# Kernel optimization log

Hardware: AMD Instinct MI355X
Metric: run time of the kernel (lower is better)

Reference implementation:

```python
import jax, jax.numpy as jnp
import numpy as np

B, S, D = 2, 2048, 1024
H, DK, DV = 16, 64, 64
DF = 4096
EPS = 1e-5


def _layer_norm(x, g, b):
    mu = jnp.mean(x, axis=-1, keepdims=True)
    var = jnp.mean((x - mu) ** 2, axis=-1, keepdims=True)
    return (x - mu) * jax.lax.rsqrt(var + EPS) * g + b


def setup_inputs() -> dict:
    key = jax.random.key(0)
    ks = jax.random.split(key, 12)
    s = lambda fan_in: 1.0 / np.sqrt(fan_in)
    return {
        "enc_input": jax.random.normal(ks[0], (B, S, D), dtype=jnp.float32),
        "wq": jax.random.uniform(ks[1], (D, H * DK), jnp.float32, -s(D), s(D)),
        "wk": jax.random.uniform(ks[2], (D, H * DK), jnp.float32, -s(D), s(D)),
        "wv": jax.random.uniform(ks[3], (D, H * DV), jnp.float32, -s(D), s(D)),
        "wo": jax.random.uniform(ks[4], (H * DV, D), jnp.float32, -s(H * DV), s(H * DV)),
        "w1": jax.random.uniform(ks[5], (D, DF), jnp.float32, -s(D), s(D)),
        "b1": jax.random.uniform(ks[6], (DF,), jnp.float32, -s(D), s(D)),
        "w2": jax.random.uniform(ks[7], (DF, D), jnp.float32, -s(DF), s(DF)),
        "b2": jax.random.uniform(ks[8], (D,), jnp.float32, -s(DF), s(DF)),
        "ln1_g": jnp.ones((D,), jnp.float32),
        "ln1_b": jnp.zeros((D,), jnp.float32),
        "ln2_g": jnp.ones((D,), jnp.float32),
        "ln2_b": jnp.zeros((D,), jnp.float32),
    }


def reference(enc_input, wq, wk, wv, wo, w1, b1, w2, b2, ln1_g, ln1_b, ln2_g, ln2_b):
    x = enc_input
    # QKV projections -> [B, H, S, d]
    q = (x @ wq).reshape(B, S, H, DK).transpose(0, 2, 1, 3)
    k = (x @ wk).reshape(B, S, H, DK).transpose(0, 2, 1, 3)
    v = (x @ wv).reshape(B, S, H, DV).transpose(0, 2, 1, 3)
    # scaled dot-product attention (scale = 1/sqrt(d_k), dropout is identity at eval)
    score = jnp.einsum("bhqd,bhkd->bhqk", q, k) / jnp.sqrt(jnp.float32(DK))
    attn = jax.nn.softmax(score, axis=-1)
    ctx = jnp.einsum("bhqk,bhkd->bhqd", attn, v)
    ctx = ctx.transpose(0, 2, 1, 3).reshape(B, S, H * DV)
    atn_out = ctx @ wo
    # Add & Norm 1
    h = _layer_norm(x + atn_out, ln1_g, ln1_b)
    # FFN
    ffn = jax.nn.relu(h @ w1 + b1) @ w2 + b2
    # Add & Norm 2
    return _layer_norm(h + ffn, ln2_g, ln2_b)
```

## Files before the change

### kernel.cpp

```cpp
#include <hip/hip_runtime.h>
#include <hip/hip_bf16.h>

typedef __bf16 bf16;
typedef __bf16 bf16x4 __attribute__((ext_vector_type(4)));
typedef __bf16 bf16x8 __attribute__((ext_vector_type(8)));
typedef float  f32x4  __attribute__((ext_vector_type(4)));

#define KB 2
#define KS 2048
#define KD 1024
#define KH 16
#define KM (KB*KS)
#define KQKVN 3072
#define KDF 4096

__device__ __forceinline__ f32x4 mfma16(bf16x8 a, bf16x8 b, f32x4 c) {
  return __builtin_amdgcn_mfma_f32_16x16x32_bf16(a, b, c, 0, 0, 0);
}

__device__ __forceinline__ void g2l16(const bf16* g, bf16* l) {
  __builtin_amdgcn_global_load_lds(
      (const __attribute__((address_space(1))) unsigned int*)g,
      (__attribute__((address_space(3))) unsigned int*)l, 16, 0, 0);
}

__global__ __launch_bounds__(256) void cvt_bf16_kernel(const float* __restrict__ in,
                                                       bf16* __restrict__ out, int n) {
  int i = (blockIdx.x * 256 + threadIdx.x) * 4;
  if (i >= n) return;
  f32x4 v = *reinterpret_cast<const f32x4*>(in + i);
  bf16x4 o;
  o[0] = (bf16)v[0]; o[1] = (bf16)v[1]; o[2] = (bf16)v[2]; o[3] = (bf16)v[3];
  *reinterpret_cast<bf16x4*>(out + i) = o;
}

__global__ __launch_bounds__(256) void wtrans_kernel(const float* __restrict__ W,
                                                     bf16* __restrict__ WT,
                                                     int K, int N) {
  __shared__ float tile[32][33];
  const int n0 = blockIdx.x * 32, k0 = blockIdx.y * 32;
  const int tx = threadIdx.x & 31, ty = threadIdx.x >> 5;
#pragma unroll
  for (int j = ty; j < 32; j += 8) tile[j][tx] = W[(size_t)(k0 + j) * N + n0 + tx];
  __syncthreads();
#pragma unroll
  for (int j = ty; j < 32; j += 8) WT[(size_t)(n0 + j) * K + k0 + tx] = (bf16)tile[tx][j];
}

__global__ __launch_bounds__(256) void kvpack_kernel(const bf16* __restrict__ qkv,
                                                     bf16* __restrict__ kp,
                                                     bf16* __restrict__ vt) {
  __shared__ bf16 tile[64][72];
  const int s0 = blockIdx.x * 64;
  const int bh = blockIdx.y;
  const int b = bh >> 4, h = bh & 15;
  const int t = threadIdx.x;
  const int r = t >> 3, c8 = (t & 7) * 8;
#pragma unroll
  for (int rr = r; rr < 64; rr += 32) {
    const size_t grow = (size_t)(b * KS + s0 + rr) * KQKVN + h * 64 + c8;
    bf16x8 kv = *reinterpret_cast<const bf16x8*>(&qkv[grow + 1024]);
    *reinterpret_cast<bf16x8*>(&kp[((size_t)bh * KS + s0 + rr) * 64 + c8]) = kv;
    bf16x8 vv = *reinterpret_cast<const bf16x8*>(&qkv[grow + 2048]);
#pragma unroll
    for (int j = 0; j < 8; j++) tile[rr][c8 + j] = vv[j];
  }
  __syncthreads();
#pragma unroll
  for (int dd = r; dd < 64; dd += 32) {
    bf16x8 v;
#pragma unroll
    for (int j = 0; j < 8; j++) {
      const int pi = c8 + j;
      v[j] = tile[((pi & 3) << 4) + (pi >> 2)][dd];
    }
    *reinterpret_cast<bf16x8*>(&vt[(size_t)bh * 64 * KS + (size_t)dd * KS + s0 + c8]) = v;
  }
}

struct P4 { bf16* p[4]; };

template <typename OUT_T, bool RELU, bool HAS_BIAS, bool SPLITK>
__global__ __launch_bounds__(512, 2) void gemm256(const bf16* __restrict__ A,
                                                  const bf16* __restrict__ BT,
                                                  OUT_T* __restrict__ C, P4 pr,
                                                  const float* __restrict__ bias,
                                                  int M, int N, int K, int Kslice) {
  extern __shared__ __align__(16) bf16 sm[];
  const int tid = threadIdx.x, lane = tid & 63, w = tid >> 6;
  const int wr = w >> 2, wc = w & 3;
  const int gx = gridDim.x;
  const int nwg = gx * gridDim.y;
  int flat = blockIdx.y * gx + blockIdx.x;
  flat = (flat & 7) * (nwg >> 3) + (flat >> 3);
  const int bn = (flat % gx) * 256;
  const int bm = (flat / gx) * 256;
  const int z = blockIdx.z;
  const int NT = (SPLITK ? Kslice : K) >> 5;
  const int lr = lane & 15, hi = lane >> 4;
  int srow[2], scol[2];
#pragma unroll
  for (int j = 0; j < 2; j++) {
    const int u = j * 512 + tid;
    srow[j] = u >> 2;
    scol[j] = (((u & 3) ^ ((u >> 2) & 3))) * 8;
  }
  const bf16* Abase = A + (size_t)bm * K + (SPLITK ? z * Kslice : 0);
  const bf16* Bbase = BT + (size_t)bn * K + (SPLITK ? z * Kslice : 0);
  auto stage = [&](int t) {
    bf16* dst = sm + (size_t)(t & 3) * 16384;
    const int k0 = t * 32;
#pragma unroll
    for (int j = 0; j < 2; j++) {
      g2l16(Abase + (size_t)srow[j] * K + k0 + scol[j], dst + (j * 512 + w * 64) * 8);
      g2l16(Bbase + (size_t)srow[j] * K + k0 + scol[j],
            dst + 8192 + (j * 512 + w * 64) * 8);
    }
  };
  f32x4 acc[8][4] = {};
  stage(0); stage(1); stage(2);
  for (int t = 0; t < NT; t++) {
    const int rem = NT - 1 - t;
    if (rem >= 2)      asm volatile("s_waitcnt vmcnt(8)" ::: "memory");
    else if (rem == 1) asm volatile("s_waitcnt vmcnt(4)" ::: "memory");
    else               asm volatile("s_waitcnt vmcnt(0)" ::: "memory");
    __builtin_amdgcn_sched_barrier(0);
    __builtin_amdgcn_s_barrier();
    __builtin_amdgcn_sched_barrier(0);
    if (t + 3 < NT) stage(t + 3);
    const bf16* sa = sm + (size_t)(t & 3) * 16384;
    const bf16* sb = sa + 8192;
    bf16x8 af[8], bfr[4];
#pragma unroll
    for (int mf = 0; mf < 8; mf++) {
      const int row = wr * 128 + mf * 16 + lr;
      af[mf] = *(const bf16x8*)&sa[row * 32 + ((hi ^ (row & 3)) * 8)];
    }
#pragma unroll
    for (int nf = 0; nf < 4; nf++) {
      const int row = wc * 64 + nf * 16 + lr;
      bfr[nf] = *(const bf16x8*)&sb[row * 32 + ((hi ^ (row & 3)) * 8)];
    }
    __builtin_amdgcn_s_setprio(1);
#pragma unroll
    for (int mf = 0; mf < 8; mf++)
#pragma unroll
      for (int nf = 0; nf < 4; nf++)
        acc[mf][nf] = mfma16(af[mf], bfr[nf], acc[mf][nf]);
    __builtin_amdgcn_s_setprio(0);
  }
  const int rg = hi * 4, cl = lr;
  if (SPLITK) {
    bf16* P = pr.p[z];
#pragma unroll
    for (int mf = 0; mf < 8; mf++)
#pragma unroll
      for (int nf = 0; nf < 4; nf++) {
        const int col = bn + wc * 64 + nf * 16 + cl;
#pragma unroll
        for (int i = 0; i < 4; i++) {
          const int row = bm + wr * 128 + mf * 16 + rg + i;
          P[(size_t)row * N + col] = (bf16)acc[mf][nf][i];
        }
      }
  } else {
#pragma unroll
    for (int mf = 0; mf < 8; mf++)
#pragma unroll
      for (int nf = 0; nf < 4; nf++) {
        const int col = bn + wc * 64 + nf * 16 + cl;
        float bv = 0.f;
        if (HAS_BIAS) bv = bias[col];
#pragma unroll
        for (int i = 0; i < 4; i++) {
          const int row = bm + wr * 128 + mf * 16 + rg + i;
          float v = acc[mf][nf][i] + bv;
          if (RELU) v = fmaxf(v, 0.f);
          C[(size_t)row * N + col] = (OUT_T)v;
        }
      }
  }
}

__global__ __launch_bounds__(256) void ffn2_reduce_kernel(const bf16* __restrict__ p0,
                                                          const bf16* __restrict__ p1,
                                                          const bf16* __restrict__ p2,
                                                          const bf16* __restrict__ p3,
                                                          const float* __restrict__ b2,
                                                          float* __restrict__ out) {
  const size_t i = ((size_t)blockIdx.x * 256 + threadIdx.x) * 8;
  bf16x8 a0 = *(const bf16x8*)(p0 + i);
  bf16x8 a1 = *(const bf16x8*)(p1 + i);
  bf16x8 a2 = *(const bf16x8*)(p2 + i);
  bf16x8 a3 = *(const bf16x8*)(p3 + i);
  const int col = (int)(i & (KD - 1));
  f32x4 b0 = *(const f32x4*)(b2 + col);
  f32x4 b1 = *(const f32x4*)(b2 + col + 4);
  f32x4 o0, o1;
#pragma unroll
  for (int j = 0; j < 4; j++)
    o0[j] = (float)a0[j] + (float)a1[j] + (float)a2[j] + (float)a3[j] + b0[j];
#pragma unroll
  for (int j = 0; j < 4; j++)
    o1[j] = (float)a0[j + 4] + (float)a1[j + 4] + (float)a2[j + 4] + (float)a3[j + 4] + b1[j];
  *(f32x4*)(out + i) = o0;
  *(f32x4*)(out + i + 4) = o1;
}

template <typename OUT_T, bool RELU, bool HAS_BIAS, int BN>
__global__ __launch_bounds__(256) void gemm_bt(const bf16* __restrict__ A,
                                               const bf16* __restrict__ BT,
                                               OUT_T* __restrict__ C,
                                               const float* __restrict__ bias,
                                               int M, int N, int K) {
  constexpr int NF = BN / 32;
  __shared__ __align__(16) bf16 sa[2][128 * 32];
  __shared__ __align__(16) bf16 sb[2][BN * 32];
  const int t = threadIdx.x, lane = t & 63, w = t >> 6;
  const int gx = gridDim.x;
  const int nwg = gx * gridDim.y;
  int flat = blockIdx.y * gx + blockIdx.x;
  if ((nwg & 7) == 0) flat = (flat & 7) * (nwg >> 3) + (flat >> 3);
  const int bn = (flat % gx) * BN;
  const int bm = (flat / gx) * 128;
  const int wr = w >> 1, wc = w & 1;
  const int wcol = wc * (BN / 2);
  const int lr = lane & 15, lk = (lane >> 4) * 8;
  const int srow = w * 16 + (lane >> 2);
  const int scol = (lane & 3) * 8;
  f32x4 acc[4][NF] = {};
  const int NT = K >> 5;
  auto stage = [&](int kt, int buf) {
#pragma unroll
    for (int i = 0; i < 2; i++)
      g2l16(A + (size_t)(bm + i * 64 + srow) * K + kt * 32 + scol,
            &sa[buf][(i * 64 + w * 16) * 32]);
#pragma unroll
    for (int i = 0; i < BN / 64; i++)
      g2l16(BT + (size_t)(bn + i * 64 + srow) * K + kt * 32 + scol,
            &sb[buf][(i * 64 + w * 16) * 32]);
  };
  stage(0, 0);
  int cur = 0;
  for (int kt = 0; kt < NT; kt++) {
    __syncthreads();
    if (kt + 1 < NT) stage(kt + 1, cur ^ 1);
    bf16x8 af[4], bfr[NF];
#pragma unroll
    for (int m = 0; m < 4; m++)
      af[m] = *(const bf16x8*)&sa[cur][(wr * 64 + m * 16 + lr) * 32 + lk];
#pragma unroll
    for (int n = 0; n < NF; n++)
      bfr[n] = *(const bf16x8*)&sb[cur][(wcol + n * 16 + lr) * 32 + lk];
#pragma unroll
    for (int m = 0; m < 4; m++)
#pragma unroll
      for (int n = 0; n < NF; n++)
        acc[m][n] = mfma16(af[m], bfr[n], acc[m][n]);
    cur ^= 1;
  }
  const int rg = (lane >> 4) * 4, cl = lane & 15;
#pragma unroll
  for (int m = 0; m < 4; m++)
#pragma unroll
    for (int n = 0; n < NF; n++) {
      const int col = bn + wcol + n * 16 + cl;
      float bv = 0.f;
      if (HAS_BIAS) bv = bias[col];
#pragma unroll
      for (int i = 0; i < 4; i++) {
        const int row = bm + wr * 64 + m * 16 + rg + i;
        float v = acc[m][n][i] + bv;
        if (RELU) v = fmaxf(v, 0.f);
        C[(size_t)row * N + col] = (OUT_T)v;
      }
    }
}

__global__ __launch_bounds__(256) void attn_kernel(const bf16* __restrict__ qkv,
                                                   const bf16* __restrict__ kp,
                                                   const bf16* __restrict__ vt,
                                                   bf16* __restrict__ ctx) {
  __shared__ __align__(16) bf16 ksm[4][64 * 64];
  __shared__ __align__(16) bf16 vsm[4][64 * 64];
  __shared__ __align__(16) bf16 psm[4][32 * 64];
  const int t = threadIdx.x, lane = t & 63, w = t >> 6;
  const int flat = blockIdx.y * 16 + blockIdx.x;
  const int xcd = flat & 7, jj = flat >> 3;
  const int bh = xcd + 8 * (jj >> 4);
  const int qb = jj & 15;
  const int b = bh >> 4, h = bh & 15;
  const int qbase = qb * 128 + w * 32;
  const int lr = lane & 15, hi = lane >> 4;
  const int lk = hi * 8, rg = hi * 4, cl = lr;

  bf16x8 aq[2][2];
#pragma unroll
  for (int m = 0; m < 2; m++)
#pragma unroll
    for (int kk = 0; kk < 2; kk++) {
      bf16x8 v = *reinterpret_cast<const bf16x8*>(
          &qkv[(size_t)(b * KS + qbase + m * 16 + lr) * KQKVN + h * 64 + kk * 32 + lk]);
#pragma unroll
      for (int e = 0; e < 8; e++) v[e] = (bf16)((float)v[e] * 0.125f);
      aq[m][kk] = v;
    }

  const bf16* kpb = kp + (size_t)bh * KS * 64;
  const bf16* vtb = vt + (size_t)bh * 64 * KS;

  auto stageKV = [&](int tt) {
    const int kt0 = tt * 64;
    bf16* kd = &ksm[tt & 3][0];
    bf16* vd = &vsm[tt & 3][0];
#pragma unroll
    for (int i = 0; i < 2; i++) {
      const int q = i * 4096 + w * 1024 + (lane << 4);
      const int row = q >> 7;
      const int slot = ((q >> 4) & 7) ^ (row & 7);
      g2l16(kpb + (size_t)(kt0 + row) * 64 + slot * 8, kd + ((i * 4096 + w * 1024) >> 1));
      g2l16(vtb + (size_t)row * KS + kt0 + slot * 8,   vd + ((i * 4096 + w * 1024) >> 1));
    }
  };

  f32x4 accd[2][4] = {};
  float lsum[2][4] = {};

  stageKV(0); stageKV(1); stageKV(2);
  char* pb = (char*)&psm[w][0];
  const int NT = KS / 64;
  for (int tt = 0; tt < NT; tt++) {
    const int rem = NT - 1 - tt;
    if (rem >= 2)      asm volatile("s_waitcnt vmcnt(8)" ::: "memory");
    else if (rem == 1) asm volatile("s_waitcnt vmcnt(4)" ::: "memory");
    else               asm volatile("s_waitcnt vmcnt(0)" ::: "memory");
    __builtin_amdgcn_sched_barrier(0);
    __builtin_amdgcn_s_barrier();
    __builtin_amdgcn_sched_barrier(0);
    if (tt + 3 < NT) stageKV(tt + 3);
    const char* kb = (const char*)&ksm[tt & 3][0];
    const char* vb = (const char*)&vsm[tt & 3][0];
    bf16x8 bk[4][2];
#pragma unroll
    for (int n = 0; n < 4; n++)
#pragma unroll
      for (int kk = 0; kk < 2; kk++) {
        const int row = n * 16 + lr;
        bk[n][kk] = *(const bf16x8*)(kb + row * 128 +
                                     ((kk * 64 + hi * 16) ^ ((row & 7) << 4)));
      }
    f32x4 sc[2][4] = {};
    __builtin_amdgcn_s_setprio(1);
#pragma unroll
    for (int m = 0; m < 2; m++)
#pragma unroll
      for (int n = 0; n < 4; n++)
#pragma unroll
        for (int kk = 0; kk < 2; kk++)
          sc[m][n] = mfma16(aq[m][kk], bk[n][kk], sc[m][n]);
    __builtin_amdgcn_s_setprio(0);
#pragma unroll
    for (int m = 0; m < 2; m++)
#pragma unroll
      for (int i = 0; i < 4; i++) {
        bf16x4 pk;
#pragma unroll
        for (int n = 0; n < 4; n++) {
          const float p = __expf(sc[m][n][i]);
          lsum[m][i] += p;
          pk[n] = (bf16)p;
        }
        const int row = m * 16 + rg + i;
        *(bf16x4*)(pb + row * 128 + ((cl * 8) ^ ((row & 7) << 4))) = pk;
      }
    bf16x8 ap[2][2];
#pragma unroll
    for (int m = 0; m < 2; m++)
#pragma unroll
      for (int kk = 0; kk < 2; kk++) {
        const int row = m * 16 + lr;
        ap[m][kk] = *(const bf16x8*)(pb + row * 128 +
                                     ((kk * 64 + hi * 16) ^ ((row & 7) << 4)));
      }
    bf16x8 bv[4][2];
#pragma unroll
    for (int dt = 0; dt < 4; dt++)
#pragma unroll
      for (int kk = 0; kk < 2; kk++) {
        const int row = dt * 16 + lr;
        bv[dt][kk] = *(const bf16x8*)(vb + row * 128 +
                                      ((kk * 64 + hi * 16) ^ ((row & 7) << 4)));
      }
    __builtin_amdgcn_s_setprio(1);
#pragma unroll
    for (int m = 0; m < 2; m++)
#pragma unroll
      for (int dt = 0; dt < 4; dt++)
#pragma unroll
        for (int kk = 0; kk < 2; kk++)
          accd[m][dt] = mfma16(ap[m][kk], bv[dt][kk], accd[m][dt]);
    __builtin_amdgcn_s_setprio(0);
  }
  float rs_[2][4];
#pragma unroll
  for (int m = 0; m < 2; m++)
#pragma unroll
    for (int i = 0; i < 4; i++) {
      float s = lsum[m][i];
#pragma unroll
      for (int off = 1; off < 16; off <<= 1) s += __shfl_xor(s, off, 64);
      rs_[m][i] = 1.0f / s;
    }
#pragma unroll
  for (int m = 0; m < 2; m++)
#pragma unroll
    for (int dt = 0; dt < 4; dt++)
#pragma unroll
      for (int i = 0; i < 4; i++)
        ctx[(size_t)(b * KS + qbase + m * 16 + rg + i) * KD + h * 64 + dt * 16 + cl] =
            (bf16)(accd[m][dt][i] * rs_[m][i]);
}

template <bool ABF, bool OBF>
__global__ __launch_bounds__(256) void ln_kernel(const void* __restrict__ aptr,
                                                 const float* __restrict__ bsum,
                                                 const float* __restrict__ g,
                                                 const float* __restrict__ bet,
                                                 void* __restrict__ outp) {
  const int row = blockIdx.x;
  const int t = threadIdx.x;
  const int lane = t & 63, wid = t >> 6;
  float v[4];
  {
    f32x4 bv = *reinterpret_cast<const f32x4*>(&bsum[(size_t)row * KD + t * 4]);
    if (ABF) {
      bf16x4 av = *reinterpret_cast<const bf16x4*>(
          (const bf16*)aptr + (size_t)row * KD + t * 4);
#pragma unroll
      for (int j = 0; j < 4; j++) v[j] = (float)av[j] + bv[j];
    } else {
      f32x4 av = *reinterpret_cast<const f32x4*>(
          (const float*)aptr + (size_t)row * KD + t * 4);
#pragma unroll
      for (int j = 0; j < 4; j++) v[j] = av[j] + bv[j];
    }
  }
  float s = 0.f, s2 = 0.f;
#pragma unroll
  for (int j = 0; j < 4; j++) { s += v[j]; s2 += v[j] * v[j]; }
#pragma unroll
  for (int off = 32; off; off >>= 1) {
    s += __shfl_xor(s, off, 64);
    s2 += __shfl_xor(s2, off, 64);
  }
  __shared__ float red[8];
  if (lane == 0) { red[wid] = s; red[wid + 4] = s2; }
  __syncthreads();
  s = red[0] + red[1] + red[2] + red[3];
  s2 = red[4] + red[5] + red[6] + red[7];
  const float mu = s * (1.f / KD);
  const float var = s2 * (1.f / KD) - mu * mu;
  const float rs = rsqrtf(var + 1e-5f);
  if (OBF) {
    bf16x4 o;
#pragma unroll
    for (int j = 0; j < 4; j++)
      o[j] = (bf16)((v[j] - mu) * rs * g[t * 4 + j] + bet[t * 4 + j]);
    *reinterpret_cast<bf16x4*>((bf16*)outp + (size_t)row * KD + t * 4) = o;
  } else {
    f32x4 o;
#pragma unroll
    for (int j = 0; j < 4; j++)
      o[j] = (v[j] - mu) * rs * g[t * 4 + j] + bet[t * 4 + j];
    *reinterpret_cast<f32x4*>((float*)outp + (size_t)row * KD + t * 4) = o;
  }
}

extern "C" void kernel_launch(void* const* d_in, const int* in_sizes, int n_in,
                              void* d_out, int out_size, void* d_ws, size_t ws_size,
                              hipStream_t stream) {
  const float* x     = (const float*)d_in[0];
  const float* wq    = (const float*)d_in[1];
  const float* wk    = (const float*)d_in[2];
  const float* wv    = (const float*)d_in[3];
  const float* wo    = (const float*)d_in[4];
  const float* w1    = (const float*)d_in[5];
  const float* b1    = (const float*)d_in[6];
  const float* w2    = (const float*)d_in[7];
  const float* b2    = (const float*)d_in[8];
  const float* ln1g  = (const float*)d_in[9];
  const float* ln1b  = (const float*)d_in[10];
  const float* ln2g  = (const float*)d_in[11];
  const float* ln2b  = (const float*)d_in[12];
  float* out = (float*)d_out;

  char* ws = (char*)d_ws;
  bf16*  x_bf   = (bf16*)(ws + 0);
  bf16*  wqkvT  = (bf16*)(ws + 8388608);
  bf16*  woT    = (bf16*)(ws + 14680064);
  bf16*  w1T    = (bf16*)(ws + 16777216);
  bf16*  w2T    = (bf16*)(ws + 25165824);
  bf16*  qkv    = (bf16*)(ws + 33554432);
  bf16*  kp     = (bf16*)(ws + 58720256);
  bf16*  vt     = (bf16*)(ws + 67108864);
  float* proj   = (float*)(ws + 75497472);
  bf16*  ctx    = x_bf;
  bf16*  h_bf   = (bf16*)(ws + 8388608);
  bf16*  ffn1   = qkv;
  float* ffn2   = (float*)(ws + 33554432);
  P4 pr;
  pr.p[0] = (bf16*)(ws + 0);
  pr.p[1] = (bf16*)(ws + 16777216);
  pr.p[2] = (bf16*)(ws + 67108864);
  pr.p[3] = (bf16*)(ws + 75497472);
  P4 pzero = {};

  cvt_bf16_kernel<<<dim3(KM * KD / 1024), 256, 0, stream>>>(x, x_bf, KM * KD);
  wtrans_kernel<<<dim3(32, 32), 256, 0, stream>>>(wq, wqkvT, KD, KD);
  wtrans_kernel<<<dim3(32, 32), 256, 0, stream>>>(wk, wqkvT + 1024 * 1024, KD, KD);
  wtrans_kernel<<<dim3(32, 32), 256, 0, stream>>>(wv, wqkvT + 2048 * 1024, KD, KD);
  wtrans_kernel<<<dim3(32, 32), 256, 0, stream>>>(wo, woT, KD, KD);
  wtrans_kernel<<<dim3(128, 32), 256, 0, stream>>>(w1, w1T, KD, KDF);
  wtrans_kernel<<<dim3(32, 128), 256, 0, stream>>>(w2, w2T, KDF, KD);

  gemm256<bf16, false, false, false>
      <<<dim3(KQKVN / 256, KM / 256, 1), 512, 131072, stream>>>(
      x_bf, wqkvT, qkv, pzero, nullptr, KM, KQKVN, KD, KD);

  kvpack_kernel<<<dim3(KS / 64, KB * KH), 256, 0, stream>>>(qkv, kp, vt);

  attn_kernel<<<dim3(KS / 128, KB * KH), 256, 0, stream>>>(qkv, kp, vt, ctx);

  gemm_bt<float, false, false, 64><<<dim3(KD / 64, KM / 128), 256, 0, stream>>>(
      ctx, woT, proj, nullptr, KM, KD, KD);

  ln_kernel<false, true><<<dim3(KM), 256, 0, stream>>>(x, proj, ln1g, ln1b, h_bf);

  gemm256<bf16, true, true, false>
      <<<dim3(KDF / 256, KM / 256, 1), 512, 131072, stream>>>(
      h_bf, w1T, ffn1, pzero, b1, KM, KDF, KD, KD);

  gemm256<bf16, false, false, true>
      <<<dim3(KD / 256, KM / 256, 4), 512, 131072, stream>>>(
      ffn1, w2T, (bf16*)nullptr, pr, nullptr, KM, KD, KDF, KDF / 4);

  ffn2_reduce_kernel<<<dim3(KM * KD / 8 / 256), 256, 0, stream>>>(
      pr.p[0], pr.p[1], pr.p[2], pr.p[3], b2, ffn2);

  ln_kernel<true, false><<<dim3(KM), 256, 0, stream>>>(h_bf, ffn2, ln2g, ln2b, out);
}
```

Before: 250.2 us.

## Keep attention probabilities in registers, use exp2 and MFMA row sums, fuse split-K reduce into LN2

The attention kernel now computes S^T by swapping the MFMA operands. This lets the exp'd probabilities be packed straight into A-operand registers, so the per-warp LDS round trip is gone. The V tile permutation is changed to match the new key ordering. Scaling folds log2(e) into Q so a raw v_exp_f32 can be used, and row sums come from an extra MFMA against a ones vector instead of shuffles. The KV pipeline drops from 4 to 3 stages, and the FFN2 split-K reduction plus bias is fused into the second layer norm, removing a kernel and a float intermediate. Risks include bf16 rounding in the row sums and no max-subtraction in the softmax, which the code before also lacked.

```diff
diff --git a/kernel.cpp b/kernel.cpp
--- a/kernel.cpp
+++ b/kernel.cpp
@@ -16,6 +16,12 @@
 
 __device__ __forceinline__ f32x4 mfma16(bf16x8 a, bf16x8 b, f32x4 c) {
   return __builtin_amdgcn_mfma_f32_16x16x32_bf16(a, b, c, 0, 0, 0);
+}
+
+__device__ __forceinline__ float exp2_hw(float x) {
+  float r;
+  asm("v_exp_f32 %0, %1" : "=v"(r) : "v"(x));
+  return r;
 }
 
 __device__ __forceinline__ void g2l16(const bf16* g, bf16* l) {
@@ -72,7 +78,9 @@
 #pragma unroll
     for (int j = 0; j < 8; j++) {
       const int pi = c8 + j;
-      v[j] = tile[((pi & 3) << 4) + (pi >> 2)][dd];
+      const int key = ((pi >> 5) << 5) | (((pi >> 2) & 1) << 4) |
+                      (((pi >> 3) & 3) << 2) | (pi & 3);
+      v[j] = tile[key][dd];
     }
     *reinterpret_cast<bf16x8*>(&vt[(size_t)bh * 64 * KS + (size_t)dd * KS + s0 + c8]) = v;
   }
@@ -180,31 +188,6 @@
         }
       }
   }
-}
-
-__global__ __launch_bounds__(256) void ffn2_reduce_kernel(const bf16* __restrict__ p0,
-                                                          const bf16* __restrict__ p1,
-                                                          const bf16* __restrict__ p2,
-                                                          const bf16* __restrict__ p3,
-                                                          const float* __restrict__ b2,
-                                                          float* __restrict__ out) {
-  const size_t i = ((size_t)blockIdx.x * 256 + threadIdx.x) * 8;
-  bf16x8 a0 = *(const bf16x8*)(p0 + i);
-  bf16x8 a1 = *(const bf16x8*)(p1 + i);
-  bf16x8 a2 = *(const bf16x8*)(p2 + i);
-  bf16x8 a3 = *(const bf16x8*)(p3 + i);
-  const int col = (int)(i & (KD - 1));
-  f32x4 b0 = *(const f32x4*)(b2 + col);
-  f32x4 b1 = *(const f32x4*)(b2 + col + 4);
-  f32x4 o0, o1;
-#pragma unroll
-  for (int j = 0; j < 4; j++)
-    o0[j] = (float)a0[j] + (float)a1[j] + (float)a2[j] + (float)a3[j] + b0[j];
-#pragma unroll
-  for (int j = 0; j < 4; j++)
-    o1[j] = (float)a0[j + 4] + (float)a1[j + 4] + (float)a2[j + 4] + (float)a3[j + 4] + b1[j];
-  *(f32x4*)(out + i) = o0;
-  *(f32x4*)(out + i + 4) = o1;
 }
 
 template <typename OUT_T, bool RELU, bool HAS_BIAS, int BN>
@@ -281,9 +264,8 @@
                                                    const bf16* __restrict__ kp,
                                                    const bf16* __restrict__ vt,
                                                    bf16* __restrict__ ctx) {
-  __shared__ __align__(16) bf16 ksm[4][64 * 64];
-  __shared__ __align__(16) bf16 vsm[4][64 * 64];
-  __shared__ __align__(16) bf16 psm[4][32 * 64];
+  __shared__ __align__(16) bf16 ksm[3][64 * 64];
+  __shared__ __align__(16) bf16 vsm[3][64 * 64];
   const int t = threadIdx.x, lane = t & 63, w = t >> 6;
   const int flat = blockIdx.y * 16 + blockIdx.x;
   const int xcd = flat & 7, jj = flat >> 3;
@@ -302,17 +284,21 @@
       bf16x8 v = *reinterpret_cast<const bf16x8*>(
           &qkv[(size_t)(b * KS + qbase + m * 16 + lr) * KQKVN + h * 64 + kk * 32 + lk]);
 #pragma unroll
-      for (int e = 0; e < 8; e++) v[e] = (bf16)((float)v[e] * 0.125f);
+      for (int e = 0; e < 8; e++) v[e] = (bf16)((float)v[e] * 0.18033688f);
       aq[m][kk] = v;
     }
+  bf16x8 ones;
+#pragma unroll
+  for (int j = 0; j < 8; j++) ones[j] = (bf16)1.0f;
 
   const bf16* kpb = kp + (size_t)bh * KS * 64;
   const bf16* vtb = vt + (size_t)bh * 64 * KS;
 
   auto stageKV = [&](int tt) {
     const int kt0 = tt * 64;
-    bf16* kd = &ksm[tt & 3][0];
-    bf16* vd = &vsm[tt & 3][0];
+    const int buf = tt % 3;
+    bf16* kd = &ksm[buf][0];
+    bf16* vd = &vsm[buf][0];
 #pragma unroll
     for (int i = 0; i < 2; i++) {
       const int q = i * 4096 + w * 1024 + (lane << 4);
@@ -324,22 +310,20 @@
   };
 
   f32x4 accd[2][4] = {};
-  float lsum[2][4] = {};
-
-  stageKV(0); stageKV(1); stageKV(2);
-  char* pb = (char*)&psm[w][0];
+  f32x4 lsumv[2] = {};
+
+  stageKV(0); stageKV(1);
   const int NT = KS / 64;
   for (int tt = 0; tt < NT; tt++) {
-    const int rem = NT - 1 - tt;
-    if (rem >= 2)      asm volatile("s_waitcnt vmcnt(8)" ::: "memory");
-    else if (rem == 1) asm volatile("s_waitcnt vmcnt(4)" ::: "memory");
-    else               asm volatile("s_waitcnt vmcnt(0)" ::: "memory");
+    if (tt < NT - 1) asm volatile("s_waitcnt vmcnt(4)" ::: "memory");
+    else             asm volatile("s_waitcnt vmcnt(0)" ::: "memory");
     __builtin_amdgcn_sched_barrier(0);
     __builtin_amdgcn_s_barrier();
     __builtin_amdgcn_sched_barrier(0);
-    if (tt + 3 < NT) stageKV(tt + 3);
-    const char* kb = (const char*)&ksm[tt & 3][0];
-    const char* vb = (const char*)&vsm[tt & 3][0];
+    if (tt + 2 < NT) stageKV(tt + 2);
+    const int buf = tt % 3;
+    const char* kb = (const char*)&ksm[buf][0];
+    const char* vb = (const char*)&vsm[buf][0];
     bf16x8 bk[4][2];
 #pragma unroll
     for (int n = 0; n < 4; n++)
@@ -357,31 +341,25 @@
       for (int n = 0; n < 4; n++)
 #pragma unroll
         for (int kk = 0; kk < 2; kk++)
-          sc[m][n] = mfma16(aq[m][kk], bk[n][kk], sc[m][n]);
+          sc[m][n] = mfma16(bk[n][kk], aq[m][kk], sc[m][n]);
     __builtin_amdgcn_s_setprio(0);
-#pragma unroll
-    for (int m = 0; m < 2; m++)
-#pragma unroll
-      for (int i = 0; i < 4; i++) {
-        bf16x4 pk;
-#pragma unroll
-        for (int n = 0; n < 4; n++) {
-          const float p = __expf(sc[m][n][i]);
-          lsum[m][i] += p;
-          pk[n] = (bf16)p;
-        }
-        const int row = m * 16 + rg + i;
-        *(bf16x4*)(pb + row * 128 + ((cl * 8) ^ ((row & 7) << 4))) = pk;
+    bf16x8 pa[2][2];
+#pragma unroll
+    for (int m = 0; m < 2; m++) {
+      float p[4][4];
+#pragma unroll
+      for (int n = 0; n < 4; n++)
+#pragma unroll
+        for (int i = 0; i < 4; i++)
+          p[n][i] = exp2_hw(sc[m][n][i]);
+#pragma unroll
+      for (int kk = 0; kk < 2; kk++) {
+        bf16x8 v;
+#pragma unroll
+        for (int j = 0; j < 8; j++) v[j] = (bf16)p[kk * 2 + (j >> 2)][j & 3];
+        pa[m][kk] = v;
       }
-    bf16x8 ap[2][2];
-#pragma unroll
-    for (int m = 0; m < 2; m++)
-#pragma unroll
-      for (int kk = 0; kk < 2; kk++) {
-        const int row = m * 16 + lr;
-        ap[m][kk] = *(const bf16x8*)(pb + row * 128 +
-                                     ((kk * 64 + hi * 16) ^ ((row & 7) << 4)));
-      }
+    }
     bf16x8 bv[4][2];
 #pragma unroll
     for (int dt = 0; dt < 4; dt++)
@@ -393,24 +371,17 @@
       }
     __builtin_amdgcn_s_setprio(1);
 #pragma unroll
-    for (int m = 0; m < 2; m++)
+    for (int m = 0; m < 2; m++) {
 #pragma unroll
       for (int dt = 0; dt < 4; dt++)
 #pragma unroll
         for (int kk = 0; kk < 2; kk++)
-          accd[m][dt] = mfma16(ap[m][kk], bv[dt][kk], accd[m][dt]);
+          accd[m][dt] = mfma16(pa[m][kk], bv[dt][kk], accd[m][dt]);
+      lsumv[m] = mfma16(pa[m][0], ones, lsumv[m]);
+      lsumv[m] = mfma16(pa[m][1], ones, lsumv[m]);
+    }
     __builtin_amdgcn_s_setprio(0);
   }
-  float rs_[2][4];
-#pragma unroll
-  for (int m = 0; m < 2; m++)
-#pragma unroll
-    for (int i = 0; i < 4; i++) {
-      float s = lsum[m][i];
-#pragma unroll
-      for (int off = 1; off < 16; off <<= 1) s += __shfl_xor(s, off, 64);
-      rs_[m][i] = 1.0f / s;
-    }
 #pragma unroll
   for (int m = 0; m < 2; m++)
 #pragma unroll
@@ -418,7 +389,7 @@
 #pragma unroll
       for (int i = 0; i < 4; i++)
         ctx[(size_t)(b * KS + qbase + m * 16 + rg + i) * KD + h * 64 + dt * 16 + cl] =
-            (bf16)(accd[m][dt][i] * rs_[m][i]);
+            (bf16)(accd[m][dt][i] / lsumv[m][i]);
 }
 
 template <bool ABF, bool OBF>
@@ -474,6 +445,52 @@
       o[j] = (v[j] - mu) * rs * g[t * 4 + j] + bet[t * 4 + j];
     *reinterpret_cast<f32x4*>((float*)outp + (size_t)row * KD + t * 4) = o;
   }
+}
+
+__global__ __launch_bounds__(256) void ln2_fused_kernel(const bf16* __restrict__ hh,
+                                                        const bf16* __restrict__ p0,
+                                                        const bf16* __restrict__ p1,
+                                                        const bf16* __restrict__ p2,
+                                                        const bf16* __restrict__ p3,
+                                                        const float* __restrict__ b2,
+                                                        const float* __restrict__ g,
+                                                        const float* __restrict__ bet,
+                                                        float* __restrict__ outp) {
+  const int row = blockIdx.x;
+  const int t = threadIdx.x;
+  const int lane = t & 63, wid = t >> 6;
+  const size_t base = (size_t)row * KD + t * 4;
+  bf16x4 hv = *(const bf16x4*)(hh + base);
+  bf16x4 a0 = *(const bf16x4*)(p0 + base);
+  bf16x4 a1 = *(const bf16x4*)(p1 + base);
+  bf16x4 a2 = *(const bf16x4*)(p2 + base);
+  bf16x4 a3 = *(const bf16x4*)(p3 + base);
+  f32x4 bv = *(const f32x4*)(b2 + t * 4);
+  float v[4];
+#pragma unroll
+  for (int j = 0; j < 4; j++)
+    v[j] = (float)hv[j] + (float)a0[j] + (float)a1[j] + (float)a2[j] + (float)a3[j] + bv[j];
+  float s = 0.f, s2 = 0.f;
+#pragma unroll
+  for (int j = 0; j < 4; j++) { s += v[j]; s2 += v[j] * v[j]; }
+#pragma unroll
+  for (int off = 32; off; off >>= 1) {
+    s += __shfl_xor(s, off, 64);
+    s2 += __shfl_xor(s2, off, 64);
+  }
+  __shared__ float red[8];
+  if (lane == 0) { red[wid] = s; red[wid + 4] = s2; }
+  __syncthreads();
+  s = red[0] + red[1] + red[2] + red[3];
+  s2 = red[4] + red[5] + red[6] + red[7];
+  const float mu = s * (1.f / KD);
+  const float var = s2 * (1.f / KD) - mu * mu;
+  const float rs = rsqrtf(var + 1e-5f);
+  f32x4 o;
+#pragma unroll
+  for (int j = 0; j < 4; j++)
+    o[j] = (v[j] - mu) * rs * g[t * 4 + j] + bet[t * 4 + j];
+  *reinterpret_cast<f32x4*>(outp + base) = o;
 }
 
 extern "C" void kernel_launch(void* const* d_in, const int* in_sizes, int n_in,
@@ -507,7 +524,6 @@
   bf16*  ctx    = x_bf;
   bf16*  h_bf   = (bf16*)(ws + 8388608);
   bf16*  ffn1   = qkv;
-  float* ffn2   = (float*)(ws + 33554432);
   P4 pr;
   pr.p[0] = (bf16*)(ws + 0);
   pr.p[1] = (bf16*)(ws + 16777216);
@@ -544,8 +560,6 @@
       <<<dim3(KD / 256, KM / 256, 4), 512, 131072, stream>>>(
       ffn1, w2T, (bf16*)nullptr, pr, nullptr, KM, KD, KDF, KDF / 4);
 
-  ffn2_reduce_kernel<<<dim3(KM * KD / 8 / 256), 256, 0, stream>>>(
-      pr.p[0], pr.p[1], pr.p[2], pr.p[3], b2, ffn2);
-
-  ln_kernel<true, false><<<dim3(KM), 256, 0, stream>>>(h_bf, ffn2, ln2g, ln2b, out);
-}
+  ln2_fused_kernel<<<dim3(KM), 256, 0, stream>>>(
+      h_bf, pr.p[0], pr.p[1], pr.p[2], pr.p[3], b2, ln2g, ln2b, out);
+}
```

Measured after the change: 241.7 us. 1.04x faster.
